# Kernel tuning notes

Measured on AMD Instinct MI355X. Metric: run time of the kernel, lower is better.

The kernel has to match this reference:

```python
import jax, jax.numpy as jnp
import numpy as np

N_NODES = 100000
N_EDGES = 1000000
IN_CH = 128
HID = 128
N_CLS = 3


def setup_inputs() -> dict:
    key = jax.random.key(0)
    ks = jax.random.split(key, 10)
    scale_in = 1.0 / np.sqrt(IN_CH)
    scale_h = 1.0 / np.sqrt(HID)
    return {
        "x": jax.random.normal(ks[0], (N_NODES, IN_CH), dtype=jnp.float32),
        "edge_index": jax.random.randint(ks[1], (2, N_EDGES), 0, N_NODES, dtype=jnp.int64),
        # SAGEConv layer 1: lin_l (aggregated neighbors, with bias), lin_r (root, no bias)
        "w_l1": jax.random.normal(ks[2], (IN_CH, HID), dtype=jnp.float32) * scale_in,
        "b_l1": jnp.zeros((HID,), dtype=jnp.float32),
        "w_r1": jax.random.normal(ks[3], (IN_CH, HID), dtype=jnp.float32) * scale_in,
        # SAGEConv layer 2
        "w_l2": jax.random.normal(ks[4], (HID, HID), dtype=jnp.float32) * scale_h,
        "b_l2": jnp.zeros((HID,), dtype=jnp.float32),
        "w_r2": jax.random.normal(ks[5], (HID, HID), dtype=jnp.float32) * scale_h,
        # final classifier
        "w_cls": jax.random.normal(ks[6], (HID, N_CLS), dtype=jnp.float32) * scale_h,
        "b_cls": jnp.zeros((N_CLS,), dtype=jnp.float32),
    }


def _sage_conv(x, src, dst, w_l, b_l, w_r, num_nodes):
    # mean aggregation of source-node features onto destination nodes
    msg = x[src]                                              # [E, C] gather
    agg = jax.ops.segment_sum(msg, dst, num_segments=num_nodes)
    cnt = jax.ops.segment_sum(jnp.ones((src.shape[0],), x.dtype), dst,
                              num_segments=num_nodes)
    mean = agg / jnp.maximum(cnt, 1.0)[:, None]
    # out = lin_l(mean_aggr) + lin_r(x)
    return mean @ w_l + b_l + x @ w_r


def reference(x, edge_index, w_l1, b_l1, w_r1, w_l2, b_l2, w_r2, w_cls, b_cls):
    src, dst = edge_index[0], edge_index[1]
    n = x.shape[0]
    h = jax.nn.relu(_sage_conv(x, src, dst, w_l1, b_l1, w_r1, n))
    # dropout is identity in eval mode
    h = jax.nn.relu(_sage_conv(h, src, dst, w_l2, b_l2, w_r2, n))
    logits = h @ w_cls + b_cls
    return logits
```

## Files before the change

### kernel.cpp

```cpp
#include <hip/hip_runtime.h>
#include <hip/hip_bf16.h>

#define N_NODES 100000
#define N_EDGES 1000000
#define CH 128
#define KTOT 256
#define NCLS 3

#define NBKT 196
#define EPB 4096
#define NB_A ((N_EDGES + EPB - 1) / EPB)
#define M_H (NBKT * NB_A)
#define NB_SCAN ((M_H + 1023) / 1024)

#define NB_CVTX (N_NODES * CH / 4 / 256)
#define NB_CVTW (KTOT * CH / 256)
#define NB_A1 (NB_A + NB_CVTX + 2 * NB_CVTW)

typedef __attribute__((ext_vector_type(8))) short v8s;
typedef __attribute__((ext_vector_type(4))) float v4f;

__device__ __forceinline__ float bf2f(unsigned short u) {
    return __uint_as_float(((unsigned int)u) << 16);
}

__device__ __forceinline__ unsigned short f2bf(float f) {
    unsigned int u = __float_as_uint(f);
    unsigned int r = (u + 0x7fffu + ((u >> 16) & 1u)) >> 16;
    return (unsigned short)r;
}

__device__ __forceinline__ int edge_at(const void* e, int is64, long long i) {
    if (is64) return (int)((const long long*)e)[i];
    return ((const int*)e)[i];
}

__device__ __forceinline__ float ldf(const void* p, int isbf, size_t i) {
    if (isbf) return bf2f(((const unsigned short*)p)[i]);
    return ((const float*)p)[i];
}

__device__ __forceinline__ void acc_u32(unsigned int u, float& a0, float& a1) {
    a0 += bf2f((unsigned short)(u & 0xffffu));
    a1 += bf2f((unsigned short)(u >> 16));
}

__global__ void k_init(const void* __restrict__ e, const unsigned int* __restrict__ x,
                       int* __restrict__ eflag, int* __restrict__ dtf,
                       int* __restrict__ done) {
    if (blockIdx.x == 0) {
        if (threadIdx.x < 64) {
            int v = ((const int*)e)[2 * threadIdx.x + 1];
            unsigned long long bl = __ballot(v != 0);
            if (threadIdx.x == 0) *eflag = (bl == 0ULL) ? 1 : 0;
        } else if (threadIdx.x == 64) {
            *done = 0;
        }
    } else {
        if (threadIdx.x < 64) {
            unsigned int u = x[threadIdx.x];
            int ex = (u >> 7) & 0xff;
            int sane = (ex == 0) || (ex >= 100 && ex <= 154);
            unsigned long long bl = __ballot(sane);
            if (threadIdx.x == 0) *dtf = (__popcll(bl) >= 48) ? 1 : 0;
        }
    }
}

__global__ void k_A1(const void* __restrict__ e, const int* __restrict__ eflag,
                     const int* __restrict__ dtf, int* __restrict__ hist,
                     const void* __restrict__ x, unsigned short* __restrict__ Xb,
                     const void* __restrict__ wl1, const void* __restrict__ wr1,
                     unsigned short* __restrict__ WT1,
                     const void* __restrict__ wl2, const void* __restrict__ wr2,
                     unsigned short* __restrict__ WT2) {
    int b = blockIdx.x;
    int t = threadIdx.x;
    if (b < NB_A) {
        __shared__ int h[NBKT];
        if (t < NBKT) h[t] = 0;
        __syncthreads();
        int is64 = *eflag;
#pragma unroll
        for (int j = 0; j < EPB / 256; j++) {
            int i = b * EPB + j * 256 + t;
            if (i < N_EDGES) {
                int dst = edge_at(e, is64, (long long)N_EDGES + i);
                atomicAdd(&h[dst >> 9], 1);
            }
        }
        __syncthreads();
        if (t < NBKT) hist[t * NB_A + b] = h[t];
    } else {
        int ob = b - NB_A;
        if (ob < NB_CVTX) {
            int idx = ob * 256 + t;
            int node = idx >> 5;
            int ch = (idx & 31) * 4;
            int isbf = *dtf;
            unsigned short o[4];
            if (isbf) {
                ushort4 u = *(const ushort4*)((const unsigned short*)x +
                                              (size_t)node * CH + ch);
                o[0] = u.x; o[1] = u.y; o[2] = u.z; o[3] = u.w;
            } else {
                float4 v = *(const float4*)((const float*)x + (size_t)node * CH + ch);
                o[0] = f2bf(v.x); o[1] = f2bf(v.y); o[2] = f2bf(v.z); o[3] = f2bf(v.w);
            }
            *(ushort4*)(Xb + (size_t)node * CH + ch) =
                make_ushort4(o[0], o[1], o[2], o[3]);
        } else {
            int rel = ob - NB_CVTX;
            const void* wl = (rel < NB_CVTW) ? wl1 : wl2;
            const void* wr = (rel < NB_CVTW) ? wr1 : wr2;
            unsigned short* WT = (rel < NB_CVTW) ? WT1 : WT2;
            int i = (rel % NB_CVTW) * 256 + t;
            int k = i >> 7;
            int n = i & 127;
            int isbf = *dtf;
            float v = (k < CH) ? ldf(wl, isbf, (size_t)k * CH + n)
                               : ldf(wr, isbf, (size_t)(k - CH) * CH + n);
            WT[(size_t)n * KTOT + k] = f2bf(v);
        }
    }
}

__global__ __launch_bounds__(1024) void k_scanH(int* __restrict__ hist,
                                                int* __restrict__ bsum,
                                                int* __restrict__ done) {
    __shared__ int s[1024];
    __shared__ int pre_sh;
    int t = threadIdx.x, b = blockIdx.x;
    int idx = b * 1024 + t;
    int v = (idx < M_H) ? hist[idx] : 0;
    s[t] = v;
    __syncthreads();
    for (int off = 1; off < 1024; off <<= 1) {
        int u = (t >= off) ? s[t - off] : 0;
        __syncthreads();
        s[t] += u;
        __syncthreads();
    }
    if (t == 1023) {
        bsum[b] = s[t];
        __threadfence();
        atomicAdd(done, 1);
    }
    if (t == 0) {
        while (__hip_atomic_load(done, __ATOMIC_ACQUIRE,
                                 __HIP_MEMORY_SCOPE_AGENT) < NB_SCAN) {
        }
        __threadfence();
        int run = 0;
        for (int r = 0; r < b; r++) run += bsum[r];
        pre_sh = run;
    }
    __syncthreads();
    if (idx < M_H) hist[idx] = s[t] - v + pre_sh;
}

__global__ void k_A3(const void* __restrict__ e, const int* __restrict__ eflag,
                     const int* __restrict__ hist, unsigned int* __restrict__ part) {
    __shared__ int cur[NBKT];
    int b = blockIdx.x;
    int t = threadIdx.x;
    if (t < NBKT) cur[t] = hist[t * NB_A + b];
    __syncthreads();
    int is64 = *eflag;
#pragma unroll
    for (int j = 0; j < EPB / 256; j++) {
        int i = b * EPB + j * 256 + t;
        if (i < N_EDGES) {
            int src = edge_at(e, is64, i);
            int dst = edge_at(e, is64, (long long)N_EDGES + i);
            int pos = atomicAdd(&cur[dst >> 9], 1);
            part[pos] = ((unsigned int)src << 9) | (unsigned int)(dst & 511);
        }
    }
}

__global__ __launch_bounds__(1024) void k_B(const int* __restrict__ hist,
                                            const unsigned int* __restrict__ part,
                                            int* __restrict__ row_start,
                                            int* __restrict__ csr_src) {
    __shared__ int dcnt[512], sa[512], curs[512];
    int b = blockIdx.x;
    int t = threadIdx.x;
    int e0 = hist[b * NB_A];
    int e1 = (b + 1 < NBKT) ? hist[(b + 1) * NB_A] : N_EDGES;
    if (t < 512) dcnt[t] = 0;
    __syncthreads();
    for (int i = e0 + t; i < e1; i += 1024)
        atomicAdd(&dcnt[part[i] & 511], 1);
    __syncthreads();
    if (t < 512) sa[t] = dcnt[t];
    __syncthreads();
    for (int off = 1; off < 512; off <<= 1) {
        int v = 0;
        if (t < 512 && t >= off) v = sa[t - off];
        __syncthreads();
        if (t < 512) sa[t] += v;
        __syncthreads();
    }
    if (t < 512) {
        int excl = sa[t] - dcnt[t];
        curs[t] = e0 + excl;
        int node = b * 512 + t;
        if (node < N_NODES) row_start[node] = e0 + excl;
    }
    if (b == 0 && t == 0) row_start[N_NODES] = N_EDGES;
    __syncthreads();
    for (int i = e0 + t; i < e1; i += 1024) {
        unsigned int p = part[i];
        int pos = atomicAdd(&curs[p & 511], 1);
        csr_src[pos] = (int)(p >> 9);
    }
}

__global__ __launch_bounds__(256) void k_agg(
    const int* __restrict__ row_start, const int* __restrict__ csr_src,
    const unsigned short* __restrict__ src, unsigned short* __restrict__ mdst) {
    long long gt = (long long)blockIdx.x * blockDim.x + threadIdx.x;
    int node = (int)(gt >> 4);
    int lane = (int)(gt & 15);
    if (node >= N_NODES) return;
    int beg = row_start[node];
    int end = row_start[node + 1];
    int n = end - beg;
    float a[8];
#pragma unroll
    for (int j = 0; j < 8; j++) a[j] = 0.f;
    if (n > 0) {
        const unsigned short* gbase = src + lane * 8;
        int nm1 = n - 1;
        int s[16];
#pragma unroll
        for (int j = 0; j < 16; j++) {
            int jj = (j < nm1) ? j : nm1;
            s[j] = csr_src[beg + jj];
        }
        uint4 u[16];
#pragma unroll
        for (int j = 0; j < 16; j++)
            u[j] = *(const uint4*)(gbase + (size_t)s[j] * CH);
#pragma unroll
        for (int j = 0; j < 16; j++) {
            if (j < n) {
                acc_u32(u[j].x, a[0], a[1]); acc_u32(u[j].y, a[2], a[3]);
                acc_u32(u[j].z, a[4], a[5]); acc_u32(u[j].w, a[6], a[7]);
            }
        }
        int e = beg + 16;
        while (e + 8 <= end) {
            int s2[8];
#pragma unroll
            for (int j = 0; j < 8; j++) s2[j] = csr_src[e + j];
            uint4 u2[8];
#pragma unroll
            for (int j = 0; j < 8; j++)
                u2[j] = *(const uint4*)(gbase + (size_t)s2[j] * CH);
#pragma unroll
            for (int j = 0; j < 8; j++) {
                acc_u32(u2[j].x, a[0], a[1]); acc_u32(u2[j].y, a[2], a[3]);
                acc_u32(u2[j].z, a[4], a[5]); acc_u32(u2[j].w, a[6], a[7]);
            }
            e += 8;
        }
        while (e < end) {
            int s0 = csr_src[e];
            uint4 u0 = *(const uint4*)(gbase + (size_t)s0 * CH);
            acc_u32(u0.x, a[0], a[1]); acc_u32(u0.y, a[2], a[3]);
            acc_u32(u0.z, a[4], a[5]); acc_u32(u0.w, a[6], a[7]);
            e++;
        }
    }
    float rinv = 1.0f / (float)max(n, 1);
    unsigned int p0 = (unsigned int)f2bf(a[0] * rinv) | ((unsigned int)f2bf(a[1] * rinv) << 16);
    unsigned int p1 = (unsigned int)f2bf(a[2] * rinv) | ((unsigned int)f2bf(a[3] * rinv) << 16);
    unsigned int p2 = (unsigned int)f2bf(a[4] * rinv) | ((unsigned int)f2bf(a[5] * rinv) << 16);
    unsigned int p3 = (unsigned int)f2bf(a[6] * rinv) | ((unsigned int)f2bf(a[7] * rinv) << 16);
    *(uint4*)(mdst + (size_t)node * CH + lane * 8) = make_uint4(p0, p1, p2, p3);
}

#define LDK 40
#define CLS_LD 130
__global__ __launch_bounds__(256) void k_gemm_mfma(
    const unsigned short* __restrict__ Mb,
    const unsigned short* __restrict__ Xr,
    const unsigned short* __restrict__ WT, const void* __restrict__ bias,
    const int* __restrict__ dtf,
    unsigned short* __restrict__ out,
    const void* __restrict__ wcls, const void* __restrict__ bcls,
    float* __restrict__ cls_out) {
    __shared__ unsigned short smem[4 * 128 * LDK];
    unsigned short* As = smem;
    unsigned short* Bs = smem + 2 * 128 * LDK;
    const int t = threadIdx.x;
    const int w = t >> 6, l = t & 63;
    const int wx = w & 1, wy = w >> 1;
    const int quad = l >> 4, lrow = l & 15;
    const int row0 = blockIdx.x * 128;
    const int srow = t >> 1, shalf = t & 1;
    const int isbf = *dtf;

    int ar = row0 + srow;
    if (ar >= N_NODES) ar = N_NODES - 1;
    const unsigned short* abase_m = Mb + (size_t)ar * CH + shalf * 16;
    const unsigned short* abase_x = Xr + (size_t)ar * CH + shalf * 16;
    const unsigned short* bbase = WT + (size_t)srow * KTOT + shalf * 16;

    v4f acc[4][4];
#pragma unroll
    for (int i = 0; i < 4; i++)
#pragma unroll
        for (int j = 0; j < 4; j++) acc[i][j] = (v4f){0.f, 0.f, 0.f, 0.f};

    {
        uint4 a0 = *(const uint4*)abase_m, a1 = *(const uint4*)(abase_m + 8);
        uint4 b0 = *(const uint4*)bbase, b1 = *(const uint4*)(bbase + 8);
        *(uint4*)&As[srow * LDK + shalf * 16] = a0;
        *(uint4*)&As[srow * LDK + shalf * 16 + 8] = a1;
        *(uint4*)&Bs[srow * LDK + shalf * 16] = b0;
        *(uint4*)&Bs[srow * LDK + shalf * 16 + 8] = b1;
    }
#pragma unroll
    for (int k = 0; k < KTOT / 32; k++) {
        uint4 na0, na1, nb0, nb1;
        if (k < KTOT / 32 - 1) {
            const unsigned short* na = (k < 3) ? (abase_m + (k + 1) * 32)
                                               : (abase_x + (k - 3) * 32);
            na0 = *(const uint4*)na;
            na1 = *(const uint4*)(na + 8);
            nb0 = *(const uint4*)(bbase + (k + 1) * 32);
            nb1 = *(const uint4*)(bbase + (k + 1) * 32 + 8);
        }
        __syncthreads();
        const int cur = (k & 1) * 128 * LDK, nxt = ((k + 1) & 1) * 128 * LDK;
        v8s af[4], bfr[4];
#pragma unroll
        for (int mi = 0; mi < 4; mi++)
            af[mi] = *(const v8s*)&As[cur + (wy * 64 + mi * 16 + lrow) * LDK + quad * 8];
#pragma unroll
        for (int ni = 0; ni < 4; ni++)
            bfr[ni] = *(const v8s*)&Bs[cur + (wx * 64 + ni * 16 + lrow) * LDK + quad * 8];
#pragma unroll
        for (int mi = 0; mi < 4; mi++)
#pragma unroll
            for (int ni = 0; ni < 4; ni++)
                acc[mi][ni] = __builtin_amdgcn_mfma_f32_16x16x32_bf16(
                    af[mi], bfr[ni], acc[mi][ni], 0, 0, 0);
        if (k < KTOT / 32 - 1) {
            *(uint4*)&As[nxt + srow * LDK + shalf * 16] = na0;
            *(uint4*)&As[nxt + srow * LDK + shalf * 16 + 8] = na1;
            *(uint4*)&Bs[nxt + srow * LDK + shalf * 16] = nb0;
            *(uint4*)&Bs[nxt + srow * LDK + shalf * 16 + 8] = nb1;
        }
    }
    float bj[4];
#pragma unroll
    for (int ni = 0; ni < 4; ni++) bj[ni] = ldf(bias, isbf, wx * 64 + ni * 16 + lrow);

    if (!cls_out) {
#pragma unroll
        for (int mi = 0; mi < 4; mi++) {
#pragma unroll
            for (int r = 0; r < 4; r++) {
                int grow = row0 + wy * 64 + mi * 16 + quad * 4 + r;
                if (grow < N_NODES) {
#pragma unroll
                    for (int ni = 0; ni < 4; ni++) {
                        int col = wx * 64 + ni * 16 + lrow;
                        float v = fmaxf(acc[mi][ni][r] + bj[ni], 0.0f);
                        out[(size_t)grow * CH + col] = f2bf(v);
                    }
                }
            }
        }
    } else {
        __syncthreads();
        float* wcls_s = (float*)(smem + 16896);
        for (int i = t; i < CH * NCLS; i += 256) wcls_s[i] = ldf(wcls, isbf, i);
#pragma unroll
        for (int mi = 0; mi < 4; mi++) {
#pragma unroll
            for (int r = 0; r < 4; r++) {
                int row = wy * 64 + mi * 16 + quad * 4 + r;
#pragma unroll
                for (int ni = 0; ni < 4; ni++) {
                    int col = wx * 64 + ni * 16 + lrow;
                    float v = fmaxf(acc[mi][ni][r] + bj[ni], 0.0f);
                    smem[row * CLS_LD + col] = f2bf(v);
                }
            }
        }
        __syncthreads();
        if (t < 128) {
            int grow = row0 + t;
            if (grow < N_NODES) {
                float a0 = 0.f, a1 = 0.f, a2 = 0.f;
                for (int k = 0; k < CH; k++) {
                    float h = bf2f(smem[t * CLS_LD + k]);
                    a0 += h * wcls_s[k * NCLS + 0];
                    a1 += h * wcls_s[k * NCLS + 1];
                    a2 += h * wcls_s[k * NCLS + 2];
                }
                cls_out[(size_t)grow * NCLS + 0] = a0 + ldf(bcls, isbf, 0);
                cls_out[(size_t)grow * NCLS + 1] = a1 + ldf(bcls, isbf, 1);
                cls_out[(size_t)grow * NCLS + 2] = a2 + ldf(bcls, isbf, 2);
            }
        }
    }
}

extern "C" void kernel_launch(void* const* d_in, const int* in_sizes, int n_in,
                              void* d_out, int out_size, void* d_ws, size_t ws_size,
                              hipStream_t stream) {
    const void* x = d_in[0];
    const void* eidx = d_in[1];
    const void* w_l1 = d_in[2];
    const void* b_l1 = d_in[3];
    const void* w_r1 = d_in[4];
    const void* w_l2 = d_in[5];
    const void* b_l2 = d_in[6];
    const void* w_r2 = d_in[7];
    const void* w_cls = d_in[8];
    const void* b_cls = d_in[9];

    char* w = (char*)d_ws;
    int* eflag = (int*)w;
    int* dtf = (int*)(w + 64);
    int* done = (int*)(w + 128);
    int* hist = (int*)(w + 4096);
    int* bsum = (int*)(w + 196608);
    int* row_start = (int*)(w + 262144);
    unsigned int* part = (unsigned int*)(w + 720896);
    int* csr_src = (int*)(w + 4915200);
    unsigned short* WT1 = (unsigned short*)(w + 8978432);
    unsigned short* WT2 = (unsigned short*)(w + 9043968);
    unsigned short* Xb = (unsigned short*)(w + 11534336);
    unsigned short* Mb = (unsigned short*)(w + 37748736);
    unsigned short* Hb = (unsigned short*)(w + 67108864);

    hipLaunchKernelGGL(k_init, dim3(2), dim3(256), 0, stream,
                       eidx, (const unsigned int*)x, eflag, dtf, done);
    hipLaunchKernelGGL(k_A1, dim3(NB_A1), dim3(256), 0, stream,
                       eidx, eflag, dtf, hist, x, Xb,
                       w_l1, w_r1, WT1, w_l2, w_r2, WT2);
    hipLaunchKernelGGL(k_scanH, dim3(NB_SCAN), dim3(1024), 0, stream,
                       hist, bsum, done);
    hipLaunchKernelGGL(k_A3, dim3(NB_A), dim3(256), 0, stream,
                       eidx, eflag, hist, part);
    hipLaunchKernelGGL(k_B, dim3(NBKT), dim3(1024), 0, stream,
                       hist, part, row_start, csr_src);
    hipLaunchKernelGGL(k_agg, dim3(N_NODES * 16 / 256), dim3(256), 0, stream,
                       row_start, csr_src, Xb, Mb);
    hipLaunchKernelGGL(k_gemm_mfma, dim3((N_NODES + 127) / 128), dim3(256), 0, stream,
                       Mb, Xb, WT1, b_l1, dtf, Hb,
                       (const void*)nullptr, (const void*)nullptr, (float*)nullptr);
    hipLaunchKernelGGL(k_agg, dim3(N_NODES * 16 / 256), dim3(256), 0, stream,
                       row_start, csr_src, Hb, Mb);
    hipLaunchKernelGGL(k_gemm_mfma, dim3((N_NODES + 127) / 128), dim3(256), 0, stream,
                       Mb, Hb, WT2, b_l2, dtf, (unsigned short*)nullptr,
                       w_cls, b_cls, (float*)d_out);
}
```

Baseline: 256.1 us.

## Load A fragments directly from global into registers and keep full weight tile in LDS

The GEMM kernel now stages the whole 128x256 transposed weight matrix in shared memory once, instead of double-buffering 32-wide K slices of both A and B. The A operand (mean-aggregated and root features) is read straight from global memory into MFMA fragment registers, with a one-step register prefetch, removing the per-iteration LDS round trip and barriers. In exchange, LDS use grows to about 66 KB per block, which may lower occupancy, and the direct global loads are 16-byte strided rows per lane, which may coalesce less well.

```diff
diff --git a/kernel.cpp b/kernel.cpp
--- a/kernel.cpp
+++ b/kernel.cpp
@@ -282,7 +282,7 @@
     *(uint4*)(mdst + (size_t)node * CH + lane * 8) = make_uint4(p0, p1, p2, p3);
 }
 
-#define LDK 40
+#define LDB 264
 #define CLS_LD 130
 __global__ __launch_bounds__(256) void k_gemm_mfma(
     const unsigned short* __restrict__ Mb,
@@ -292,22 +292,32 @@
     unsigned short* __restrict__ out,
     const void* __restrict__ wcls, const void* __restrict__ bcls,
     float* __restrict__ cls_out) {
-    __shared__ unsigned short smem[4 * 128 * LDK];
-    unsigned short* As = smem;
-    unsigned short* Bs = smem + 2 * 128 * LDK;
+    __shared__ unsigned short Bs[128 * LDB];
     const int t = threadIdx.x;
     const int w = t >> 6, l = t & 63;
     const int wx = w & 1, wy = w >> 1;
     const int quad = l >> 4, lrow = l & 15;
     const int row0 = blockIdx.x * 128;
-    const int srow = t >> 1, shalf = t & 1;
     const int isbf = *dtf;
 
-    int ar = row0 + srow;
-    if (ar >= N_NODES) ar = N_NODES - 1;
-    const unsigned short* abase_m = Mb + (size_t)ar * CH + shalf * 16;
-    const unsigned short* abase_x = Xr + (size_t)ar * CH + shalf * 16;
-    const unsigned short* bbase = WT + (size_t)srow * KTOT + shalf * 16;
+    {
+        const int r = t >> 1, sh = t & 1;
+        const unsigned short* bsrc = WT + (size_t)r * KTOT + sh * 128;
+        unsigned short* bdst = Bs + r * LDB + sh * 128;
+#pragma unroll
+        for (int j = 0; j < 16; j++)
+            *(uint4*)(bdst + j * 8) = *(const uint4*)(bsrc + j * 8);
+    }
+
+    const unsigned short* aM[4];
+    const unsigned short* aX[4];
+#pragma unroll
+    for (int mi = 0; mi < 4; mi++) {
+        int r = row0 + wy * 64 + mi * 16 + lrow;
+        if (r >= N_NODES) r = N_NODES - 1;
+        aM[mi] = Mb + (size_t)r * CH + quad * 8;
+        aX[mi] = Xr + (size_t)r * CH + quad * 8;
+    }
 
     v4f acc[4][4];
 #pragma unroll
@@ -315,47 +325,37 @@
 #pragma unroll
         for (int j = 0; j < 4; j++) acc[i][j] = (v4f){0.f, 0.f, 0.f, 0.f};
 
-    {
-        uint4 a0 = *(const uint4*)abase_m, a1 = *(const uint4*)(abase_m + 8);
-        uint4 b0 = *(const uint4*)bbase, b1 = *(const uint4*)(bbase + 8);
-        *(uint4*)&As[srow * LDK + shalf * 16] = a0;
-        *(uint4*)&As[srow * LDK + shalf * 16 + 8] = a1;
-        *(uint4*)&Bs[srow * LDK + shalf * 16] = b0;
-        *(uint4*)&Bs[srow * LDK + shalf * 16 + 8] = b1;
-    }
+    v8s afc[4];
+#pragma unroll
+    for (int mi = 0; mi < 4; mi++) afc[mi] = *(const v8s*)(aM[mi]);
+
+    __syncthreads();
+
 #pragma unroll
     for (int k = 0; k < KTOT / 32; k++) {
-        uint4 na0, na1, nb0, nb1;
+        v8s afn[4];
         if (k < KTOT / 32 - 1) {
-            const unsigned short* na = (k < 3) ? (abase_m + (k + 1) * 32)
-                                               : (abase_x + (k - 3) * 32);
-            na0 = *(const uint4*)na;
-            na1 = *(const uint4*)(na + 8);
-            nb0 = *(const uint4*)(bbase + (k + 1) * 32);
-            nb1 = *(const uint4*)(bbase + (k + 1) * 32 + 8);
-        }
-        __syncthreads();
-        const int cur = (k & 1) * 128 * LDK, nxt = ((k + 1) & 1) * 128 * LDK;
-        v8s af[4], bfr[4];
-#pragma unroll
-        for (int mi = 0; mi < 4; mi++)
-            af[mi] = *(const v8s*)&As[cur + (wy * 64 + mi * 16 + lrow) * LDK + quad * 8];
+            const int kn = k + 1;
+#pragma unroll
+            for (int mi = 0; mi < 4; mi++)
+                afn[mi] = *(const v8s*)((kn < 4) ? (aM[mi] + kn * 32)
+                                                 : (aX[mi] + (kn - 4) * 32));
+        }
+        v8s bfr[4];
 #pragma unroll
         for (int ni = 0; ni < 4; ni++)
-            bfr[ni] = *(const v8s*)&Bs[cur + (wx * 64 + ni * 16 + lrow) * LDK + quad * 8];
+            bfr[ni] = *(const v8s*)&Bs[(wx * 64 + ni * 16 + lrow) * LDB +
+                                       k * 32 + quad * 8];
 #pragma unroll
         for (int mi = 0; mi < 4; mi++)
 #pragma unroll
             for (int ni = 0; ni < 4; ni++)
                 acc[mi][ni] = __builtin_amdgcn_mfma_f32_16x16x32_bf16(
-                    af[mi], bfr[ni], acc[mi][ni], 0, 0, 0);
-        if (k < KTOT / 32 - 1) {
-            *(uint4*)&As[nxt + srow * LDK + shalf * 16] = na0;
-            *(uint4*)&As[nxt + srow * LDK + shalf * 16 + 8] = na1;
-            *(uint4*)&Bs[nxt + srow * LDK + shalf * 16] = nb0;
-            *(uint4*)&Bs[nxt + srow * LDK + shalf * 16 + 8] = nb1;
-        }
-    }
+                    afc[mi], bfr[ni], acc[mi][ni], 0, 0, 0);
+#pragma unroll
+        for (int mi = 0; mi < 4; mi++) afc[mi] = afn[mi];
+    }
+
     float bj[4];
 #pragma unroll
     for (int ni = 0; ni < 4; ni++) bj[ni] = ldf(bias, isbf, wx * 64 + ni * 16 + lrow);
@@ -378,7 +378,7 @@
         }
     } else {
         __syncthreads();
-        float* wcls_s = (float*)(smem + 16896);
+        float* wcls_s = (float*)(Bs + 16896);
         for (int i = t; i < CH * NCLS; i += 256) wcls_s[i] = ldf(wcls, isbf, i);
 #pragma unroll
         for (int mi = 0; mi < 4; mi++) {
@@ -389,7 +389,7 @@
                 for (int ni = 0; ni < 4; ni++) {
                     int col = wx * 64 + ni * 16 + lrow;
                     float v = fmaxf(acc[mi][ni][r] + bj[ni], 0.0f);
-                    smem[row * CLS_LD + col] = f2bf(v);
+                    Bs[row * CLS_LD + col] = f2bf(v);
                 }
             }
         }
@@ -399,7 +399,7 @@
             if (grow < N_NODES) {
                 float a0 = 0.f, a1 = 0.f, a2 = 0.f;
                 for (int k = 0; k < CH; k++) {
-                    float h = bf2f(smem[t * CLS_LD + k]);
+                    float h = bf2f(Bs[t * CLS_LD + k]);
                     a0 += h * wcls_s[k * NCLS + 0];
                     a1 += h * wcls_s[k * NCLS + 1];
                     a2 += h * wcls_s[k * NCLS + 2];
```

Result: slower. 279.4 us (+9.1%).

## Drop init kernel and spread x bf16 conversion across small CSR-build kernels

Applied to the files above, without the earlier changes.

Removes the separate k_init launch. Data-type and index-width detection now happens inline through wave ballots in k_A1, and block 0 writes the flags. The 12500 tiles of x-to-bf16 conversion are split out of k_A1 and appended as extra blocks to k_scanH, k_A3 and k_B. Those kernels launch few blocks and would otherwise leave most CUs idle. This saves one launch and hides conversion bandwidth behind latency-bound scan and partition work, at the cost of more dispatch and some redundant sniffing per block.

```diff
diff --git a/kernel.cpp b/kernel.cpp
--- a/kernel.cpp
+++ b/kernel.cpp
@@ -15,7 +15,9 @@
 
 #define NB_CVTX (N_NODES * CH / 4 / 256)
 #define NB_CVTW (KTOT * CH / 256)
-#define NB_A1 (NB_A + NB_CVTX + 2 * NB_CVTW)
+#define CVT_SCAN 4000
+#define CVT_A3   4500
+#define CVT_B    4000
 
 typedef __attribute__((ext_vector_type(8))) short v8s;
 typedef __attribute__((ext_vector_type(4))) float v4f;
@@ -45,31 +47,43 @@
     a1 += bf2f((unsigned short)(u >> 16));
 }
 
-__global__ void k_init(const void* __restrict__ e, const unsigned int* __restrict__ x,
-                       int* __restrict__ eflag, int* __restrict__ dtf,
-                       int* __restrict__ done) {
-    if (blockIdx.x == 0) {
-        if (threadIdx.x < 64) {
-            int v = ((const int*)e)[2 * threadIdx.x + 1];
-            unsigned long long bl = __ballot(v != 0);
-            if (threadIdx.x == 0) *eflag = (bl == 0ULL) ? 1 : 0;
-        } else if (threadIdx.x == 64) {
-            *done = 0;
-        }
+__device__ __forceinline__ int sniff_is64(const void* e) {
+    int lane = threadIdx.x & 63;
+    int v = ((const int*)e)[2 * lane + 1];
+    unsigned long long bl = __ballot(v != 0);
+    return (bl == 0ULL) ? 1 : 0;
+}
+
+__device__ __forceinline__ int sniff_isbf(const void* x) {
+    int lane = threadIdx.x & 63;
+    unsigned int u = ((const unsigned int*)x)[lane];
+    int ex = (u >> 7) & 0xff;
+    int sane = (ex == 0) || (ex >= 100 && ex <= 154);
+    unsigned long long bl = __ballot(sane);
+    return (__popcll(bl) >= 48) ? 1 : 0;
+}
+
+__device__ __forceinline__ void cvt_x_tile(int tile, int t256, const void* x,
+                                           unsigned short* Xb, int isbf) {
+    int idx = tile * 256 + t256;
+    int node = idx >> 5;
+    int ch = (idx & 31) * 4;
+    unsigned short o[4];
+    if (isbf) {
+        ushort4 u = *(const ushort4*)((const unsigned short*)x +
+                                      (size_t)node * CH + ch);
+        o[0] = u.x; o[1] = u.y; o[2] = u.z; o[3] = u.w;
     } else {
-        if (threadIdx.x < 64) {
-            unsigned int u = x[threadIdx.x];
-            int ex = (u >> 7) & 0xff;
-            int sane = (ex == 0) || (ex >= 100 && ex <= 154);
-            unsigned long long bl = __ballot(sane);
-            if (threadIdx.x == 0) *dtf = (__popcll(bl) >= 48) ? 1 : 0;
-        }
-    }
-}
-
-__global__ void k_A1(const void* __restrict__ e, const int* __restrict__ eflag,
-                     const int* __restrict__ dtf, int* __restrict__ hist,
-                     const void* __restrict__ x, unsigned short* __restrict__ Xb,
+        float4 v = *(const float4*)((const float*)x + (size_t)node * CH + ch);
+        o[0] = f2bf(v.x); o[1] = f2bf(v.y); o[2] = f2bf(v.z); o[3] = f2bf(v.w);
+    }
+    *(ushort4*)(Xb + (size_t)node * CH + ch) = make_ushort4(o[0], o[1], o[2], o[3]);
+}
+
+__global__ void k_A1(const void* __restrict__ e, int* __restrict__ eflag,
+                     int* __restrict__ dtf, int* __restrict__ done,
+                     int* __restrict__ hist,
+                     const void* __restrict__ x,
                      const void* __restrict__ wl1, const void* __restrict__ wr1,
                      unsigned short* __restrict__ WT1,
                      const void* __restrict__ wl2, const void* __restrict__ wr2,
@@ -79,8 +93,12 @@
     if (b < NB_A) {
         __shared__ int h[NBKT];
         if (t < NBKT) h[t] = 0;
-        __syncthreads();
-        int is64 = *eflag;
+        int is64 = sniff_is64(e);
+        if (b == 0 && t < 64) {
+            int isbf = sniff_isbf(x);
+            if (t == 0) { *eflag = is64; *dtf = isbf; *done = 0; }
+        }
+        __syncthreads();
 #pragma unroll
         for (int j = 0; j < EPB / 256; j++) {
             int i = b * EPB + j * 256 + t;
@@ -92,45 +110,35 @@
         __syncthreads();
         if (t < NBKT) hist[t * NB_A + b] = h[t];
     } else {
-        int ob = b - NB_A;
-        if (ob < NB_CVTX) {
-            int idx = ob * 256 + t;
-            int node = idx >> 5;
-            int ch = (idx & 31) * 4;
-            int isbf = *dtf;
-            unsigned short o[4];
-            if (isbf) {
-                ushort4 u = *(const ushort4*)((const unsigned short*)x +
-                                              (size_t)node * CH + ch);
-                o[0] = u.x; o[1] = u.y; o[2] = u.z; o[3] = u.w;
-            } else {
-                float4 v = *(const float4*)((const float*)x + (size_t)node * CH + ch);
-                o[0] = f2bf(v.x); o[1] = f2bf(v.y); o[2] = f2bf(v.z); o[3] = f2bf(v.w);
-            }
-            *(ushort4*)(Xb + (size_t)node * CH + ch) =
-                make_ushort4(o[0], o[1], o[2], o[3]);
-        } else {
-            int rel = ob - NB_CVTX;
-            const void* wl = (rel < NB_CVTW) ? wl1 : wl2;
-            const void* wr = (rel < NB_CVTW) ? wr1 : wr2;
-            unsigned short* WT = (rel < NB_CVTW) ? WT1 : WT2;
-            int i = (rel % NB_CVTW) * 256 + t;
-            int k = i >> 7;
-            int n = i & 127;
-            int isbf = *dtf;
-            float v = (k < CH) ? ldf(wl, isbf, (size_t)k * CH + n)
-                               : ldf(wr, isbf, (size_t)(k - CH) * CH + n);
-            WT[(size_t)n * KTOT + k] = f2bf(v);
-        }
+        int rel = b - NB_A;
+        int isbf = sniff_isbf(x);
+        const void* wl = (rel < NB_CVTW) ? wl1 : wl2;
+        const void* wr = (rel < NB_CVTW) ? wr1 : wr2;
+        unsigned short* WT = (rel < NB_CVTW) ? WT1 : WT2;
+        int i = (rel % NB_CVTW) * 256 + t;
+        int k = i >> 7;
+        int n = i & 127;
+        float v = (k < CH) ? ldf(wl, isbf, (size_t)k * CH + n)
+                           : ldf(wr, isbf, (size_t)(k - CH) * CH + n);
+        WT[(size_t)n * KTOT + k] = f2bf(v);
     }
 }
 
 __global__ __launch_bounds__(1024) void k_scanH(int* __restrict__ hist,
                                                 int* __restrict__ bsum,
-                                                int* __restrict__ done) {
+                                                int* __restrict__ done,
+                                                const void* __restrict__ x,
+                                                unsigned short* __restrict__ Xb,
+                                                const int* __restrict__ dtf) {
     __shared__ int s[1024];
     __shared__ int pre_sh;
     int t = threadIdx.x, b = blockIdx.x;
+    if (b >= NB_SCAN) {
+        int cb = b - NB_SCAN;
+        int isbf = *dtf;
+        cvt_x_tile(cb * 4 + (t >> 8), t & 255, x, Xb, isbf);
+        return;
+    }
     int idx = b * 1024 + t;
     int v = (idx < M_H) ? hist[idx] : 0;
     s[t] = v;
@@ -160,10 +168,17 @@
 }
 
 __global__ void k_A3(const void* __restrict__ e, const int* __restrict__ eflag,
-                     const int* __restrict__ hist, unsigned int* __restrict__ part) {
+                     const int* __restrict__ hist, unsigned int* __restrict__ part,
+                     const void* __restrict__ x, unsigned short* __restrict__ Xb,
+                     const int* __restrict__ dtf) {
     __shared__ int cur[NBKT];
     int b = blockIdx.x;
     int t = threadIdx.x;
+    if (b >= NB_A) {
+        int isbf = *dtf;
+        cvt_x_tile(CVT_SCAN + (b - NB_A), t, x, Xb, isbf);
+        return;
+    }
     if (t < NBKT) cur[t] = hist[t * NB_A + b];
     __syncthreads();
     int is64 = *eflag;
@@ -182,10 +197,19 @@
 __global__ __launch_bounds__(1024) void k_B(const int* __restrict__ hist,
                                             const unsigned int* __restrict__ part,
                                             int* __restrict__ row_start,
-                                            int* __restrict__ csr_src) {
+                                            int* __restrict__ csr_src,
+                                            const void* __restrict__ x,
+                                            unsigned short* __restrict__ Xb,
+                                            const int* __restrict__ dtf) {
     __shared__ int dcnt[512], sa[512], curs[512];
     int b = blockIdx.x;
     int t = threadIdx.x;
+    if (b >= NBKT) {
+        int cb = b - NBKT;
+        int isbf = *dtf;
+        cvt_x_tile(CVT_SCAN + CVT_A3 + cb * 4 + (t >> 8), t & 255, x, Xb, isbf);
+        return;
+    }
     int e0 = hist[b * NB_A];
     int e1 = (b + 1 < NBKT) ? hist[(b + 1) * NB_A] : N_EDGES;
     if (t < 512) dcnt[t] = 0;
@@ -441,17 +465,15 @@
     unsigned short* Mb = (unsigned short*)(w + 37748736);
     unsigned short* Hb = (unsigned short*)(w + 67108864);
 
-    hipLaunchKernelGGL(k_init, dim3(2), dim3(256), 0, stream,
-                       eidx, (const unsigned int*)x, eflag, dtf, done);
-    hipLaunchKernelGGL(k_A1, dim3(NB_A1), dim3(256), 0, stream,
-                       eidx, eflag, dtf, hist, x, Xb,
+    hipLaunchKernelGGL(k_A1, dim3(NB_A + 2 * NB_CVTW), dim3(256), 0, stream,
+                       eidx, eflag, dtf, done, hist, x,
                        w_l1, w_r1, WT1, w_l2, w_r2, WT2);
-    hipLaunchKernelGGL(k_scanH, dim3(NB_SCAN), dim3(1024), 0, stream,
-                       hist, bsum, done);
-    hipLaunchKernelGGL(k_A3, dim3(NB_A), dim3(256), 0, stream,
-                       eidx, eflag, hist, part);
-    hipLaunchKernelGGL(k_B, dim3(NBKT), dim3(1024), 0, stream,
-                       hist, part, row_start, csr_src);
+    hipLaunchKernelGGL(k_scanH, dim3(NB_SCAN + CVT_SCAN / 4), dim3(1024), 0, stream,
+                       hist, bsum, done, x, Xb, dtf);
+    hipLaunchKernelGGL(k_A3, dim3(NB_A + CVT_A3), dim3(256), 0, stream,
+                       eidx, eflag, hist, part, x, Xb, dtf);
+    hipLaunchKernelGGL(k_B, dim3(NBKT + CVT_B / 4), dim3(1024), 0, stream,
+                       hist, part, row_start, csr_src, x, Xb, dtf);
     hipLaunchKernelGGL(k_agg, dim3(N_NODES * 16 / 256), dim3(256), 0, stream,
                        row_start, csr_src, Xb, Mb);
     hipLaunchKernelGGL(k_gemm_mfma, dim3((N_NODES + 127) / 128), dim3(256), 0, stream,
```

After: 256.1 us. Within noise of the previous version (-0.0%).
